# Kernel tuning notes

Measured on AMD Instinct MI355X. Metric: run time of the kernel, lower is better.

## Reference

```python
import jax, jax.numpy as jnp
import numpy as np

EMBED_DIM = 1024
NUM_HEADS = 16
HEAD_DIM = EMBED_DIM // NUM_HEADS


def setup_inputs() -> dict:
    key = jax.random.key(0)
    ks = jax.random.split(key, 11)
    B, N, C = 2, 2048, EMBED_DIM
    s = 1.0 / np.sqrt(C)
    return {
        "query": jax.random.normal(ks[0], (B, N, C), jnp.float32),
        "key": jax.random.normal(ks[1], (B, N, C), jnp.float32),
        "value": jax.random.normal(ks[2], (B, N, C), jnp.float32),
        # torch nn.Linear weights: [out_features, in_features]
        "Wq": jax.random.normal(ks[3], (C, C), jnp.float32) * s,
        "bq": jnp.zeros((C,), jnp.float32),
        "Wk": jax.random.normal(ks[4], (C, C), jnp.float32) * s,
        "bk": jnp.zeros((C,), jnp.float32),
        "Wv": jax.random.normal(ks[5], (C, C), jnp.float32) * s,
        "bv": jnp.zeros((C,), jnp.float32),
        "Wo": jax.random.normal(ks[6], (C, C), jnp.float32) * s,
        "bo": jnp.zeros((C,), jnp.float32),
    }


def reference(query, key, value, Wq, bq, Wk, bk, Wv, bv, Wo, bo):
    B, N, C = query.shape
    H, D = NUM_HEADS, HEAD_DIM
    # projections (torch Linear: x @ W.T + b)
    q = query @ Wq.T + bq
    k = key @ Wk.T + bk
    v = value @ Wv.T + bv
    # [B, N, C] -> [B, H, N, D]
    q = q.reshape(B, N, H, D).transpose(0, 2, 1, 3)
    k = k.reshape(B, N, H, D).transpose(0, 2, 1, 3)
    v = v.reshape(B, N, H, D).transpose(0, 2, 1, 3)
    # scores: [B, H, N, N]
    scores = jnp.einsum("bhqd,bhkd->bhqk", q, k) / jnp.sqrt(jnp.asarray(D, q.dtype))
    attn = jax.nn.softmax(scores, axis=-1)
    # attend: [B, H, N, D] -> [B, N, C]
    out = jnp.einsum("bhqk,bhkd->bhqd", attn, v)
    out = out.transpose(0, 2, 1, 3).reshape(B, N, C)
    return out @ Wo.T + bo
```

## Files before the change

### kernel.cpp

```cpp
#include <hip/hip_runtime.h>
#include <hip/hip_bf16.h>
#include <cstdint>

typedef short bf16x8 __attribute__((ext_vector_type(8)));
typedef float f32x4 __attribute__((ext_vector_type(4)));
typedef float f32x16 __attribute__((ext_vector_type(16)));
typedef uint32_t u32x4v __attribute__((ext_vector_type(4)));
typedef unsigned short u16;

#define BATCH 2
#define NTOK 2048
#define CDIM 1024
#define NHEAD 16
#define DHEAD 64
#define MROWS 4096
#define KDIM 1024
#define KVB 128
#define NT (NTOK / KVB)

__device__ __forceinline__ uint32_t packbf2(float lo, float hi) {
    float2 f; f.x = lo; f.y = hi;
    __hip_bfloat162 h = __float22bfloat162_rn(f);
    uint32_t r;
    __builtin_memcpy(&r, &h, 4);
    return r;
}

__device__ __forceinline__ u16 f2bf(float x) {
    return (u16)(packbf2(x, 0.f) & 0xffffu);
}

__device__ __forceinline__ void gload_lds16(const void* g, void* l) {
    __builtin_amdgcn_global_load_lds((const __attribute__((address_space(1))) void*)g,
                                     (__attribute__((address_space(3))) void*)l,
                                     16, 0, 0);
}

__global__ __launch_bounds__(256) void cast_kernel(
    const float* __restrict__ q, const float* __restrict__ k, const float* __restrict__ v,
    const float* __restrict__ wq, const float* __restrict__ wk, const float* __restrict__ wv,
    const float* __restrict__ wo, u16* __restrict__ dst) {
    const size_t TOT = 16u << 20;
    size_t i0 = ((size_t)blockIdx.x * 256 + threadIdx.x) * 4;
    size_t stride = (size_t)gridDim.x * 256 * 4;
    for (size_t i = i0; i < TOT; i += stride) {
        const float* src;
        size_t off = i;
        if (i < (4u << 20))        { src = q;  }
        else if (i < (8u << 20))   { src = k;  off = i - (4u << 20); }
        else if (i < (12u << 20))  { src = v;  off = i - (8u << 20); }
        else if (i < (13u << 20))  { src = wq; off = i - (12u << 20); }
        else if (i < (14u << 20))  { src = wk; off = i - (13u << 20); }
        else if (i < (15u << 20))  { src = wv; off = i - (14u << 20); }
        else                       { src = wo; off = i - (15u << 20); }
        float4 f = *(const float4*)(src + off);
        uint2 packed;
        packed.x = packbf2(f.x, f.y);
        packed.y = packbf2(f.z, f.w);
        *(uint2*)(dst + i) = packed;
    }
}

__global__ __launch_bounds__(256, 3) void gemm_qkv(
    const u16* __restrict__ Xq, const u16* __restrict__ Xk, const u16* __restrict__ Xv,
    const u16* __restrict__ Wq, const u16* __restrict__ Wk, const u16* __restrict__ Wv,
    const float* __restrict__ bq, const float* __restrict__ bk, const float* __restrict__ bv,
    u16* __restrict__ Qo, u16* __restrict__ Ko, u16* __restrict__ Vo) {
    __shared__ u16 sA[128 * 64];
    __shared__ u16 sB[128 * 64];
    const int tid = threadIdx.x;
    const int lane = tid & 63;
    const int wave = tid >> 6;
    const int z = blockIdx.z;
    const u16* A  = (z == 0) ? Xq : (z == 1) ? Xk : Xv;
    const u16* Bw = (z == 0) ? Wq : (z == 1) ? Wk : Wv;
    const float* bias = (z == 0) ? bq : (z == 1) ? bk : bv;
    u16* Out = (z == 0) ? Qo : (z == 1) ? Ko : Vo;
    const float scale = (z == 0) ? 0.125f * 1.44269504088896f : 1.0f;

    const int m0 = blockIdx.x * 128, n0 = blockIdx.y * 128;
    const int wm = (wave >> 1) * 64, wn = (wave & 1) * 64;
    f32x4 acc[4][4] = {};
    const int rsel = lane & 15;
    const int g = lane >> 4;

    for (int k0 = 0; k0 < KDIM; k0 += 64) {
#pragma unroll
        for (int u = 0; u < 4; ++u) {
            int c2 = tid + u * 256;
            int row = c2 >> 3, gi = c2 & 7;
            int sc = (gi ^ (row & 7)) * 8;
            gload_lds16(A + (size_t)(m0 + row) * KDIM + k0 + sc, &sA[c2 * 8]);
            gload_lds16(Bw + (size_t)(n0 + row) * KDIM + k0 + sc, &sB[c2 * 8]);
        }
        __syncthreads();
        bf16x8 af[4][2], bfr[4][2];
#pragma unroll
        for (int i = 0; i < 4; ++i) {
            int r = wm + i * 16 + rsel;
#pragma unroll
            for (int h2 = 0; h2 < 2; ++h2)
                af[i][h2] = *(const bf16x8*)&sA[r * 64 + (((g + 4 * h2) ^ (r & 7)) * 8)];
        }
#pragma unroll
        for (int j = 0; j < 4; ++j) {
            int r = wn + j * 16 + rsel;
#pragma unroll
            for (int h2 = 0; h2 < 2; ++h2)
                bfr[j][h2] = *(const bf16x8*)&sB[r * 64 + (((g + 4 * h2) ^ (r & 7)) * 8)];
        }
#pragma unroll
        for (int i = 0; i < 4; ++i)
#pragma unroll
            for (int j = 0; j < 4; ++j)
#pragma unroll
                for (int h2 = 0; h2 < 2; ++h2)
                    acc[i][j] = __builtin_amdgcn_mfma_f32_16x16x32_bf16(af[i][h2], bfr[j][h2], acc[i][j], 0, 0, 0);
        __syncthreads();
    }

    if (z != 2) {
#pragma unroll
        for (int i = 0; i < 4; ++i) {
            int mbase = m0 + wm + i * 16 + (lane >> 4) * 4;
#pragma unroll
            for (int j = 0; j < 4; ++j) {
                int n = n0 + wn + j * 16 + (lane & 15);
                float bv2 = bias[n];
                int h = n >> 6, d = n & 63;
#pragma unroll
                for (int r = 0; r < 4; ++r) {
                    int m = mbase + r;
                    int b = m >> 11, tok = m & 2047;
                    Out[(((size_t)(b * NHEAD + h)) * NTOK + tok) * DHEAD + d] =
                        f2bf((acc[i][j][r] + bv2) * scale);
                }
            }
        }
    } else {
#pragma unroll
        for (int i = 0; i < 4; ++i) {
            int mbase = m0 + wm + i * 16 + (lane >> 4) * 4;
            int b = mbase >> 11, tok = mbase & 2047;
#pragma unroll
            for (int j = 0; j < 4; ++j) {
                int n = n0 + wn + j * 16 + (lane & 15);
                float bv2 = bias[n];
                int h = n >> 6, d = n & 63;
                uint2 st;
                st.x = packbf2(acc[i][j][0] + bv2, acc[i][j][1] + bv2);
                st.y = packbf2(acc[i][j][2] + bv2, acc[i][j][3] + bv2);
                *(uint2*)&Out[(((size_t)(b * NHEAD + h)) * DHEAD + d) * NTOK + tok] = st;
            }
        }
    }
}

__global__ __launch_bounds__(256, 3) void gemm_out(
    const u16* __restrict__ A,
    const u16* __restrict__ Bw,
    const float* __restrict__ bias,
    float* __restrict__ Out,
    int M, int N, int K) {
    __shared__ u16 sA[128 * 64];
    __shared__ u16 sB[128 * 64];
    const int tid = threadIdx.x;
    const int lane = tid & 63;
    const int wave = tid >> 6;
    const int m0 = blockIdx.x * 128, n0 = blockIdx.y * 128;
    const int wm = (wave >> 1) * 64, wn = (wave & 1) * 64;
    f32x4 acc[4][4] = {};
    const int rsel = lane & 15;
    const int g = lane >> 4;

    for (int k0 = 0; k0 < K; k0 += 64) {
#pragma unroll
        for (int u = 0; u < 4; ++u) {
            int c2 = tid + u * 256;
            int row = c2 >> 3, gi = c2 & 7;
            int sc = (gi ^ (row & 7)) * 8;
            gload_lds16(A + (size_t)(m0 + row) * K + k0 + sc, &sA[c2 * 8]);
            gload_lds16(Bw + (size_t)(n0 + row) * K + k0 + sc, &sB[c2 * 8]);
        }
        __syncthreads();
        bf16x8 af[4][2], bfr[4][2];
#pragma unroll
        for (int i = 0; i < 4; ++i) {
            int r = wm + i * 16 + rsel;
#pragma unroll
            for (int h2 = 0; h2 < 2; ++h2)
                af[i][h2] = *(const bf16x8*)&sA[r * 64 + (((g + 4 * h2) ^ (r & 7)) * 8)];
        }
#pragma unroll
        for (int j = 0; j < 4; ++j) {
            int r = wn + j * 16 + rsel;
#pragma unroll
            for (int h2 = 0; h2 < 2; ++h2)
                bfr[j][h2] = *(const bf16x8*)&sB[r * 64 + (((g + 4 * h2) ^ (r & 7)) * 8)];
        }
#pragma unroll
        for (int i = 0; i < 4; ++i)
#pragma unroll
            for (int j = 0; j < 4; ++j)
#pragma unroll
                for (int h2 = 0; h2 < 2; ++h2)
                    acc[i][j] = __builtin_amdgcn_mfma_f32_16x16x32_bf16(af[i][h2], bfr[j][h2], acc[i][j], 0, 0, 0);
        __syncthreads();
    }

#pragma unroll
    for (int i = 0; i < 4; ++i) {
        int mbase = m0 + wm + i * 16 + (lane >> 4) * 4;
#pragma unroll
        for (int j = 0; j < 4; ++j) {
            int n = n0 + wn + j * 16 + (lane & 15);
            float bv = bias[n];
#pragma unroll
            for (int r = 0; r < 4; ++r) {
                int m = mbase + r;
                Out[(size_t)m * N + n] = acc[i][j][r] + bv;
            }
        }
    }
}

__global__ __launch_bounds__(256, 2) void attn_kernel(
    const u16* __restrict__ Qg, const u16* __restrict__ Kg, const u16* __restrict__ Vg,
    u16* __restrict__ Og) {
    __shared__ u16 Ks[2][KVB * 64];
    __shared__ u16 Vt[2][64 * KVB];
    const int tid = threadIdx.x, lane = tid & 63, wave = tid >> 6;
    const int hi = lane >> 5, lq = lane & 31;

    int flat = blockIdx.x;
    int vflat = (flat & 7) * 64 + (flat >> 3);
    int bh = vflat >> 4;
    int qtile = vflat & 15;

    const int h = bh & (NHEAD - 1), b = bh >> 4;
    const u16* Qh = Qg + (size_t)bh * NTOK * DHEAD;
    const u16* Kh = Kg + (size_t)bh * NTOK * DHEAD;
    const u16* VhT = Vg + (size_t)bh * DHEAD * NTOK;
    const int qrow0 = qtile * 128 + wave * 32;
    const int qr = qrow0 + lq;

    bf16x8 qf[4];
#pragma unroll
    for (int dk = 0; dk < 4; ++dk)
        qf[dk] = *(const bf16x8*)&Qh[(size_t)qr * DHEAD + dk * 16 + hi * 8];

    f32x16 acc0 = {}, acc1 = {};
    float lrun = 0.f;

    const int pr = ((lq >> 2) & 1) * 8 + (lq & 3) + ((lq >> 3) & 1) * 4 + (lq >> 4) * 16;

    {
#pragma unroll
        for (int u = 0; u < 4; ++u) {
            int c2 = tid + u * 256;
            int kv = c2 >> 3, gi = c2 & 7;
            gload_lds16(Kh + (size_t)kv * DHEAD + (gi ^ (kv & 7)) * 8, &Ks[0][c2 * 8]);
        }
#pragma unroll
        for (int u = 0; u < 4; ++u) {
            int c2 = tid + u * 256;
            int d = c2 >> 4, gi = c2 & 15;
            gload_lds16(VhT + (size_t)d * NTOK + (gi ^ (d & 15)) * 8, &Vt[0][c2 * 8]);
        }
    }
    __syncthreads();

    int cur = 0;
    for (int t = 0; t < NT; ++t) {
        const bool pre = (t + 1 < NT);
        if (pre) {
#pragma unroll
            for (int u = 0; u < 4; ++u) {
                int c2 = tid + u * 256;
                int kv = c2 >> 3, gi = c2 & 7;
                gload_lds16(Kh + (size_t)((t + 1) * KVB + kv) * DHEAD + (gi ^ (kv & 7)) * 8,
                            &Ks[cur ^ 1][c2 * 8]);
            }
#pragma unroll
            for (int u = 0; u < 4; ++u) {
                int c2 = tid + u * 256;
                int d = c2 >> 4, gi = c2 & 15;
                gload_lds16(VhT + (size_t)d * NTOK + (t + 1) * KVB + (gi ^ (d & 15)) * 8,
                            &Vt[cur ^ 1][c2 * 8]);
            }
        }

        const char* kb_ = (const char*)&Ks[cur][0];
        bf16x8 pf[8];
        float smv[16];
#pragma unroll
        for (int i = 0; i < 16; ++i) smv[i] = 0.f;
#pragma unroll
        for (int j = 0; j < 4; ++j) {
            f32x16 T = {};
            int kv = j * 32 + pr;
            const char* kr = kb_ + kv * 128;
            int sx = (kv & 7) << 4;
#pragma unroll
            for (int dk = 0; dk < 4; ++dk) {
                bf16x8 kf = *(const bf16x8*)(kr + ((dk * 32 + hi * 16) ^ sx));
                T = __builtin_amdgcn_mfma_f32_32x32x16_bf16(kf, qf[dk], T, 0, 0, 0);
            }
#pragma unroll
            for (int i = 0; i < 16; ++i) T[i] = __builtin_amdgcn_exp2f(T[i]);
#pragma unroll
            for (int i = 0; i < 16; ++i) smv[i] += T[i];
            u32x4v w0 = { packbf2(T[0], T[1]),  packbf2(T[2], T[3]),
                          packbf2(T[4], T[5]),  packbf2(T[6], T[7]) };
            u32x4v w1 = { packbf2(T[8], T[9]),  packbf2(T[10], T[11]),
                          packbf2(T[12], T[13]), packbf2(T[14], T[15]) };
            pf[j * 2]     = *(bf16x8*)&w0;
            pf[j * 2 + 1] = *(bf16x8*)&w1;
        }

        const char* vb_ = (const char*)&Vt[cur][0];
        __builtin_amdgcn_s_setprio(1);
#pragma unroll
        for (int db = 0; db < 2; ++db) {
            int d = db * 32 + lq;
#pragma unroll
            for (int ks = 0; ks < 8; ++ks) {
                int off = d * 256 + ((ks * 32 + hi * 16) ^ ((d & 15) << 4));
                bf16x8 vf = *(const bf16x8*)(vb_ + off);
                if (db == 0)
                    acc0 = __builtin_amdgcn_mfma_f32_32x32x16_bf16(vf, pf[ks], acc0, 0, 0, 0);
                else
                    acc1 = __builtin_amdgcn_mfma_f32_32x32x16_bf16(vf, pf[ks], acc1, 0, 0, 0);
            }
        }
        __builtin_amdgcn_s_setprio(0);

#pragma unroll
        for (int s2 = 8; s2 >= 1; s2 >>= 1)
#pragma unroll
            for (int i = 0; i < s2; ++i) smv[i] += smv[i + s2];
        lrun += smv[0] + __shfl_xor(smv[0], 32);

        __syncthreads();
        cur ^= 1;
    }

    float rinv = 1.0f / lrun;
#pragma unroll
    for (int db = 0; db < 2; ++db) {
#pragma unroll
        for (int rq = 0; rq < 4; ++rq) {
            int based = db * 32 + 8 * rq + 4 * hi;
            float o0, o1, o2, o3;
            if (db == 0) {
                o0 = acc0[rq * 4 + 0]; o1 = acc0[rq * 4 + 1];
                o2 = acc0[rq * 4 + 2]; o3 = acc0[rq * 4 + 3];
            } else {
                o0 = acc1[rq * 4 + 0]; o1 = acc1[rq * 4 + 1];
                o2 = acc1[rq * 4 + 2]; o3 = acc1[rq * 4 + 3];
            }
            uint2 st;
            st.x = packbf2(o0 * rinv, o1 * rinv);
            st.y = packbf2(o2 * rinv, o3 * rinv);
            *(uint2*)&Og[((size_t)(b * NTOK + qr)) * CDIM + h * DHEAD + based] = st;
        }
    }
}

extern "C" void kernel_launch(void* const* d_in, const int* in_sizes, int n_in,
                              void* d_out, int out_size, void* d_ws, size_t ws_size,
                              hipStream_t stream) {
    const float* q  = (const float*)d_in[0];
    const float* k  = (const float*)d_in[1];
    const float* v  = (const float*)d_in[2];
    const float* Wq = (const float*)d_in[3];
    const float* bq = (const float*)d_in[4];
    const float* Wk = (const float*)d_in[5];
    const float* bk = (const float*)d_in[6];
    const float* Wv = (const float*)d_in[7];
    const float* bv = (const float*)d_in[8];
    const float* Wo = (const float*)d_in[9];
    const float* bo = (const float*)d_in[10];

    u16* wsp = (u16*)d_ws;
    u16* Xq  = wsp;
    u16* Xk  = Xq + (4u << 20);
    u16* Xv  = Xk + (4u << 20);
    u16* Wqb = Xv + (4u << 20);
    u16* Wkb = Wqb + (1u << 20);
    u16* Wvb = Wkb + (1u << 20);
    u16* Wob = Wvb + (1u << 20);
    u16* Qb  = Wob + (1u << 20);
    u16* Kb  = Qb + (4u << 20);
    u16* Vb  = Kb + (4u << 20);
    u16* Ab  = Xq;

    cast_kernel<<<2048, 256, 0, stream>>>(q, k, v, Wq, Wk, Wv, Wo, Xq);

    gemm_qkv<<<dim3(MROWS / 128, CDIM / 128, 3), 256, 0, stream>>>(
        Xq, Xk, Xv, Wqb, Wkb, Wvb, bq, bk, bv, Qb, Kb, Vb);

    attn_kernel<<<512, 256, 0, stream>>>(Qb, Kb, Vb, Ab);

    gemm_out<<<dim3(MROWS / 128, CDIM / 128), 256, 0, stream>>>(
        Ab, Wob, bo, (float*)d_out, MROWS, CDIM, KDIM);
}
```

Baseline: 118.0 us.

## Software-pipeline attention loop so QK^T of next tile overlaps PV of current

Result: no change. 119.3 us (+1.1%).

```diff
diff --git a/kernel.cpp b/kernel.cpp
--- a/kernel.cpp
+++ b/kernel.cpp
@@ -254,44 +254,35 @@
 
     const int pr = ((lq >> 2) & 1) * 8 + (lq & 3) + ((lq >> 3) & 1) * 4 + (lq >> 4) * 16;
 
+#define STAGE_K(TT, BUF)                                                              \
+    {                                                                                 \
+        _Pragma("unroll")                                                             \
+        for (int u = 0; u < 4; ++u) {                                                 \
+            int c2 = tid + u * 256;                                                   \
+            int kv = c2 >> 3, gi = c2 & 7;                                            \
+            gload_lds16(Kh + (size_t)((TT) * KVB + kv) * DHEAD + (gi ^ (kv & 7)) * 8, \
+                        &Ks[BUF][c2 * 8]);                                            \
+        }                                                                             \
+    }
+#define STAGE_V(TT, BUF)                                                              \
+    {                                                                                 \
+        _Pragma("unroll")                                                             \
+        for (int u = 0; u < 4; ++u) {                                                 \
+            int c2 = tid + u * 256;                                                   \
+            int d = c2 >> 4, gi = c2 & 15;                                            \
+            gload_lds16(VhT + (size_t)d * NTOK + (TT) * KVB + (gi ^ (d & 15)) * 8,    \
+                        &Vt[BUF][c2 * 8]);                                            \
+        }                                                                             \
+    }
+
+    STAGE_K(0, 0);
+    STAGE_V(0, 0);
+    __syncthreads();
+    STAGE_K(1, 1);
+
+    bf16x8 pf[8];
     {
-#pragma unroll
-        for (int u = 0; u < 4; ++u) {
-            int c2 = tid + u * 256;
-            int kv = c2 >> 3, gi = c2 & 7;
-            gload_lds16(Kh + (size_t)kv * DHEAD + (gi ^ (kv & 7)) * 8, &Ks[0][c2 * 8]);
-        }
-#pragma unroll
-        for (int u = 0; u < 4; ++u) {
-            int c2 = tid + u * 256;
-            int d = c2 >> 4, gi = c2 & 15;
-            gload_lds16(VhT + (size_t)d * NTOK + (gi ^ (d & 15)) * 8, &Vt[0][c2 * 8]);
-        }
-    }
-    __syncthreads();
-
-    int cur = 0;
-    for (int t = 0; t < NT; ++t) {
-        const bool pre = (t + 1 < NT);
-        if (pre) {
-#pragma unroll
-            for (int u = 0; u < 4; ++u) {
-                int c2 = tid + u * 256;
-                int kv = c2 >> 3, gi = c2 & 7;
-                gload_lds16(Kh + (size_t)((t + 1) * KVB + kv) * DHEAD + (gi ^ (kv & 7)) * 8,
-                            &Ks[cur ^ 1][c2 * 8]);
-            }
-#pragma unroll
-            for (int u = 0; u < 4; ++u) {
-                int c2 = tid + u * 256;
-                int d = c2 >> 4, gi = c2 & 15;
-                gload_lds16(VhT + (size_t)d * NTOK + (t + 1) * KVB + (gi ^ (d & 15)) * 8,
-                            &Vt[cur ^ 1][c2 * 8]);
-            }
-        }
-
-        const char* kb_ = (const char*)&Ks[cur][0];
-        bf16x8 pf[8];
+        const char* kb_ = (const char*)&Ks[0][0];
         float smv[16];
 #pragma unroll
         for (int i = 0; i < 16; ++i) smv[i] = 0.f;
@@ -317,8 +308,75 @@
             pf[j * 2]     = *(bf16x8*)&w0;
             pf[j * 2 + 1] = *(bf16x8*)&w1;
         }
-
-        const char* vb_ = (const char*)&Vt[cur][0];
+#pragma unroll
+        for (int s2 = 8; s2 >= 1; s2 >>= 1)
+#pragma unroll
+            for (int i = 0; i < s2; ++i) smv[i] += smv[i + s2];
+        lrun += smv[0] + __shfl_xor(smv[0], 32);
+    }
+    __syncthreads();
+
+    for (int t = 0; t < NT - 1; ++t) {
+        if (t + 2 < NT) STAGE_K(t + 2, t & 1);
+        STAGE_V(t + 1, (t + 1) & 1);
+
+        const char* kb_ = (const char*)&Ks[(t + 1) & 1][0];
+        const char* vb_ = (const char*)&Vt[t & 1][0];
+        bf16x8 pfn[8];
+        float smv[16];
+#pragma unroll
+        for (int i = 0; i < 16; ++i) smv[i] = 0.f;
+
+        __builtin_amdgcn_s_setprio(1);
+#pragma unroll
+        for (int j = 0; j < 4; ++j) {
+            f32x16 T = {};
+            int kv = j * 32 + pr;
+            const char* kr = kb_ + kv * 128;
+            int sx = (kv & 7) << 4;
+#pragma unroll
+            for (int dk = 0; dk < 4; ++dk) {
+                bf16x8 kf = *(const bf16x8*)(kr + ((dk * 32 + hi * 16) ^ sx));
+                T = __builtin_amdgcn_mfma_f32_32x32x16_bf16(kf, qf[dk], T, 0, 0, 0);
+            }
+            {
+                int d0 = lq, d1 = 32 + lq;
+#pragma unroll
+                for (int kk = 0; kk < 2; ++kk) {
+                    int ks = j * 2 + kk;
+                    int xo = (ks * 32 + hi * 16);
+                    bf16x8 vf0 = *(const bf16x8*)(vb_ + d0 * 256 + (xo ^ ((d0 & 15) << 4)));
+                    bf16x8 vf1 = *(const bf16x8*)(vb_ + d1 * 256 + (xo ^ ((d1 & 15) << 4)));
+                    acc0 = __builtin_amdgcn_mfma_f32_32x32x16_bf16(vf0, pf[ks], acc0, 0, 0, 0);
+                    acc1 = __builtin_amdgcn_mfma_f32_32x32x16_bf16(vf1, pf[ks], acc1, 0, 0, 0);
+                }
+            }
+#pragma unroll
+            for (int i = 0; i < 16; ++i) T[i] = __builtin_amdgcn_exp2f(T[i]);
+#pragma unroll
+            for (int i = 0; i < 16; ++i) smv[i] += T[i];
+            u32x4v w0 = { packbf2(T[0], T[1]),  packbf2(T[2], T[3]),
+                          packbf2(T[4], T[5]),  packbf2(T[6], T[7]) };
+            u32x4v w1 = { packbf2(T[8], T[9]),  packbf2(T[10], T[11]),
+                          packbf2(T[12], T[13]), packbf2(T[14], T[15]) };
+            pfn[j * 2]     = *(bf16x8*)&w0;
+            pfn[j * 2 + 1] = *(bf16x8*)&w1;
+        }
+        __builtin_amdgcn_s_setprio(0);
+
+#pragma unroll
+        for (int s2 = 8; s2 >= 1; s2 >>= 1)
+#pragma unroll
+            for (int i = 0; i < s2; ++i) smv[i] += smv[i + s2];
+        lrun += smv[0] + __shfl_xor(smv[0], 32);
+
+        __syncthreads();
+#pragma unroll
+        for (int i = 0; i < 8; ++i) pf[i] = pfn[i];
+    }
+
+    {
+        const char* vb_ = (const char*)&Vt[(NT - 1) & 1][0];
         __builtin_amdgcn_s_setprio(1);
 #pragma unroll
         for (int db = 0; db < 2; ++db) {
@@ -334,15 +392,6 @@
             }
         }
         __builtin_amdgcn_s_setprio(0);
-
-#pragma unroll
-        for (int s2 = 8; s2 >= 1; s2 >>= 1)
-#pragma unroll
-            for (int i = 0; i < s2; ++i) smv[i] += smv[i + s2];
-        lrun += smv[0] + __shfl_xor(smv[0], 32);
-
-        __syncthreads();
-        cur ^= 1;
     }
 
     float rinv = 1.0f / lrun;
@@ -365,6 +414,8 @@
             *(uint2*)&Og[((size_t)(b * NTOK + qr)) * CDIM + h * DHEAD + based] = st;
         }
     }
+#undef STAGE_K
+#undef STAGE_V
 }
 
 extern "C" void kernel_launch(void* const* d_in, const int* in_sizes, int n_in,
```
